# Optimization experiments

Measured on AMD Instinct MI355X. Metric: run time of the kernel, lower is better.

The kernel has to match this reference:

```python
import jax, jax.numpy as jnp
import numpy as np

B, N, DIM = 256, 196, 384
H, KD, VD = 12, 32, 32
RES = 14
EPS = 1e-5


def _build_bias_idxs():
    pts = [(i, j) for i in range(RES) for j in range(RES)]
    offs, idxs = {}, []
    for p1 in pts:
        for p2 in pts:
            o = (abs(p1[0] - p2[0]), abs(p1[1] - p2[1]))
            if o not in offs:
                offs[o] = len(offs)
            idxs.append(offs[o])
    return jnp.asarray(np.array(idxs, dtype=np.int32).reshape(N, N))


def setup_inputs() -> dict:
    key = jax.random.key(0)
    ks = jax.random.split(key, 4)
    return {
        "x": jax.random.normal(ks[0], (B, N, DIM), dtype=jnp.float32),
        "norm_w": jnp.ones((DIM,), jnp.float32),
        "norm_b": jnp.zeros((DIM,), jnp.float32),
        "qkv_w": jax.random.normal(ks[1], (H * (VD + 2 * KD), DIM), jnp.float32) * 0.02,
        "qkv_b": jnp.zeros((H * (VD + 2 * KD),), jnp.float32),
        "attention_biases": jax.random.normal(ks[2], (H, RES * RES), jnp.float32) * 0.02,
        "proj_w": jax.random.normal(ks[3], (DIM, H * VD), jnp.float32) * 0.02,
        "proj_b": jnp.zeros((DIM,), jnp.float32),
        "bias_idxs": _build_bias_idxs(),
    }


def reference(x, norm_w, norm_b, qkv_w, qkv_b, attention_biases, proj_w, proj_b, bias_idxs):
    scale = KD ** -0.5
    # LayerNorm over feature dim
    mu = jnp.mean(x, axis=-1, keepdims=True)
    var = jnp.mean(jnp.square(x - mu), axis=-1, keepdims=True)
    xn = (x - mu) * jax.lax.rsqrt(var + EPS) * norm_w + norm_b
    # QKV projection: [B,N,H*(2*KD+VD)] -> [B,N,H,*]
    qkv = (jnp.einsum("bnd,fd->bnf", xn, qkv_w) + qkv_b).reshape(B, N, H, 2 * KD + VD)
    q, k, v = qkv[..., :KD], qkv[..., KD:2 * KD], qkv[..., 2 * KD:]
    # Relative-position bias gathered into [H,N,N]
    attn_bias = attention_biases[:, bias_idxs]
    # Scores [B,H,N,N] with bias, softmax, AV
    scores = jnp.einsum("bnhk,bmhk->bhnm", q * scale, k) + attn_bias
    probs = jax.nn.softmax(scores, axis=-1)
    out = jnp.einsum("bhnm,bmhv->bnhv", probs, v).reshape(B, N, H * VD)
    return jnp.einsum("bnf,df->bnd", out, proj_w) + proj_b
```

## Files before the change

### kernel.cpp

```cpp
#include <hip/hip_runtime.h>

#define B_    256
#define N_    196
#define NP_   208
#define VSTR_ 264
#define DIM_  384
#define H_    12
#define KD_   32
#define VD_   32
#define F_    1152
#define ROWS_ (B_ * N_)
#define SCALE_ 0.17677669529663687f
#define EPS_  1e-5f

typedef __bf16 bf16_t;
typedef __bf16 bf16x2 __attribute__((ext_vector_type(2)));
typedef __bf16 bf16x4 __attribute__((ext_vector_type(4)));
typedef __bf16 bf16x8 __attribute__((ext_vector_type(8)));
typedef float  f32x4  __attribute__((ext_vector_type(4)));

__device__ __forceinline__ f32x4 mfma16(bf16x8 a, bf16x8 b, f32x4 c) {
    return __builtin_amdgcn_mfma_f32_16x16x32_bf16(a, b, c, 0, 0, 0);
}

__device__ __forceinline__ void gl2lds(const bf16_t* g, bf16_t* l) {
    __builtin_amdgcn_global_load_lds(
        (const __attribute__((address_space(1))) void*)g,
        (__attribute__((address_space(3))) void*)l, 16, 0, 0);
}

__global__ __launch_bounds__(256) void cvt_w(const float* __restrict__ src,
                                             bf16_t* __restrict__ dst) {
    const int i = (blockIdx.x * 256 + threadIdx.x) * 4;
    const float4 v = *(const float4*)(src + i);
    bf16x4 o = {(bf16_t)v.x, (bf16_t)v.y, (bf16_t)v.z, (bf16_t)v.w};
    *(bf16x4*)(dst + i) = o;
}

__global__ __launch_bounds__(256) void ln_kernel(const float* __restrict__ x,
                                                 const float* __restrict__ w,
                                                 const float* __restrict__ bvec,
                                                 bf16_t* __restrict__ xn) {
    const int lane = threadIdx.x & 63;
    const int row  = blockIdx.x * 4 + (threadIdx.x >> 6);
    const float* xr = x + (size_t)row * DIM_;
    const float4 a = *(const float4*)(xr + lane * 4);
    const float2 c = *(const float2*)(xr + 256 + lane * 2);
    float s  = a.x + a.y + a.z + a.w + c.x + c.y;
    float s2 = a.x*a.x + a.y*a.y + a.z*a.z + a.w*a.w + c.x*c.x + c.y*c.y;
    #pragma unroll
    for (int o = 32; o > 0; o >>= 1) {
        s  += __shfl_xor(s, o);
        s2 += __shfl_xor(s2, o);
    }
    const float mu = s * (1.f / 384.f);
    const float rs = rsqrtf(s2 * (1.f / 384.f) - mu * mu + EPS_);
    const float4 w4 = *(const float4*)(w + lane * 4);
    const float2 w2 = *(const float2*)(w + 256 + lane * 2);
    const float4 b4 = *(const float4*)(bvec + lane * 4);
    const float2 b2 = *(const float2*)(bvec + 256 + lane * 2);
    bf16_t* orow = xn + (size_t)row * DIM_;
    bf16x4 o4 = {(bf16_t)((a.x - mu) * rs * w4.x + b4.x),
                 (bf16_t)((a.y - mu) * rs * w4.y + b4.y),
                 (bf16_t)((a.z - mu) * rs * w4.z + b4.z),
                 (bf16_t)((a.w - mu) * rs * w4.w + b4.w)};
    *(bf16x4*)(orow + lane * 4) = o4;
    bf16x2 o2 = {(bf16_t)((c.x - mu) * rs * w2.x + b2.x),
                 (bf16_t)((c.y - mu) * rs * w2.y + b2.y)};
    *(bf16x2*)(orow + 256 + lane * 2) = o2;
}

__global__ __launch_bounds__(256) void bias_gather(const float* __restrict__ biases,
                                                   const int* __restrict__ idxs,
                                                   bf16_t* __restrict__ biasmat) {
    const int e = blockIdx.x * 256 + threadIdx.x;
    if (e >= H_ * N_ * NP_) return;
    const int h = e / (N_ * NP_);
    const int r = e % (N_ * NP_);
    const int n = r / NP_;
    const int m = r % NP_;
    const float v = (m < N_) ? biases[h * N_ + idxs[n * N_ + m]] : -1e30f;
    biasmat[e] = (bf16_t)v;
}

template <typename OutT>
__global__ __launch_bounds__(256) void gemm_mfma(const bf16_t* __restrict__ A,
                                                 const bf16_t* __restrict__ Wt,
                                                 const float* __restrict__ bias,
                                                 OutT* __restrict__ C,
                                                 int M, int Nout, int K) {
    __shared__ __align__(16) bf16_t As[128][32];
    __shared__ __align__(16) bf16_t Bs[128][32];
    const int tid  = threadIdx.x;
    const int lane = tid & 63;
    const int wv   = tid >> 6;
    const int ln   = lane & 15;
    const int ko   = lane >> 4;
    const int wr   = (wv >> 1) * 64;
    const int wc   = (wv & 1) * 64;
    const size_t bm = (size_t)blockIdx.x * 128;
    const size_t bn = (size_t)blockIdx.y * 128;

    const int srow = wv * 16 + (lane >> 2);
    const int scol = (lane & 3) * 8;
    const bf16_t* gA0 = A  + (bm + srow) * K + scol;
    const bf16_t* gA1 = gA0 + (size_t)64 * K;
    const bf16_t* gB0 = Wt + (bn + srow) * K + scol;
    const bf16_t* gB1 = gB0 + (size_t)64 * K;
    bf16_t* lA0 = &As[srow][scol];
    bf16_t* lA1 = &As[srow + 64][scol];
    bf16_t* lB0 = &Bs[srow][scol];
    bf16_t* lB1 = &Bs[srow + 64][scol];

    f32x4 acc[4][4];
    #pragma unroll
    for (int i = 0; i < 4; i++)
        #pragma unroll
        for (int j = 0; j < 4; j++)
            acc[i][j] = (f32x4){0.f, 0.f, 0.f, 0.f};

    for (int k0 = 0; k0 < K; k0 += 32) {
        gl2lds(gA0 + k0, lA0);
        gl2lds(gA1 + k0, lA1);
        gl2lds(gB0 + k0, lB0);
        gl2lds(gB1 + k0, lB1);
        __syncthreads();
        bf16x8 af[4], bfr[4];
        #pragma unroll
        for (int i = 0; i < 4; i++)
            af[i] = *(const bf16x8*)&As[wr + i * 16 + ln][ko * 8];
        #pragma unroll
        for (int j = 0; j < 4; j++)
            bfr[j] = *(const bf16x8*)&Bs[wc + j * 16 + ln][ko * 8];
        #pragma unroll
        for (int i = 0; i < 4; i++)
            #pragma unroll
            for (int j = 0; j < 4; j++)
                acc[i][j] = mfma16(af[i], bfr[j], acc[i][j]);
        __syncthreads();
    }

    #pragma unroll
    for (int j = 0; j < 4; j++) {
        const size_t col = bn + wc + j * 16 + ln;
        const float bcol = bias[col];
        #pragma unroll
        for (int i = 0; i < 4; i++)
            #pragma unroll
            for (int r = 0; r < 4; r++) {
                const size_t row = bm + wr + i * 16 + ko * 4 + r;
                C[row * Nout + col] = (OutT)(acc[i][j][r] + bcol);
            }
    }
}

__global__ __launch_bounds__(256) void attn_mfma(const bf16_t* __restrict__ qkv,
                                                 const bf16_t* __restrict__ biasmat,
                                                 bf16_t* __restrict__ out) {
    const int b = blockIdx.x / H_;
    const int h = blockIdx.x % H_;
    __shared__ __align__(16) bf16_t Ks[NP_][32];
    __shared__ __align__(16) bf16_t Vt[VD_][VSTR_];
    __shared__ __align__(16) bf16_t Pb[4][16][VSTR_];
    const int tid  = threadIdx.x;
    const int lane = tid & 63;
    const int wv   = tid >> 6;
    const int ln   = lane & 15;
    const int ko   = lane >> 4;

    {
        const int rsub = lane >> 2;
        const int col  = (lane & 3) * 8;
        for (int c = wv; c < 13; c += 4) {
            const int row = c * 16 + rsub;
            gl2lds(qkv + ((size_t)(b * N_ + row) * H_ + h) * 96 + KD_ + col,
                   &Ks[row][col]);
        }
    }
    if (tid < 224) {
        const int m  = tid;
        const int kk = (m & 15) * 16 + (m >> 4);
        const bf16_t* src = qkv + ((size_t)(b * N_ + m) * H_ + h) * 96 + 2 * KD_;
        #pragma unroll
        for (int c4 = 0; c4 < 4; c4++) {
            bf16x8 v8 = {bf16_t(0), bf16_t(0), bf16_t(0), bf16_t(0),
                         bf16_t(0), bf16_t(0), bf16_t(0), bf16_t(0)};
            if (m < N_) v8 = *(const bf16x8*)(src + c4 * 8);
            #pragma unroll
            for (int j = 0; j < 8; j++) Vt[c4 * 8 + j][kk] = v8[j];
        }
    }
    for (int e = tid; e < 32 * 32; e += 256) {
        const int v = e >> 5;
        const int s = e & 31;
        Vt[v][(s >> 1) * 16 + 14 + (s & 1)] = bf16_t(0);
    }
    __syncthreads();

    bf16x8 kf[13];
    #pragma unroll
    for (int c = 0; c < 13; c++)
        kf[c] = *(const bf16x8*)&Ks[c * 16 + ln][ko * 8];

    for (int t = wv; t < 13; t += 4) {
        const int qrow = t * 16 + ln;
        const bf16x8 qf =
            *(const bf16x8*)(qkv + ((size_t)(b * N_ + qrow) * H_ + h) * 96 + ko * 8);

        f32x4 sc[13];
        #pragma unroll
        for (int c = 0; c < 13; c++) {
            f32x4 z = {0.f, 0.f, 0.f, 0.f};
            sc[c] = mfma16(qf, kf[c], z);
        }

        float mx[4] = {-1e30f, -1e30f, -1e30f, -1e30f};
        #pragma unroll
        for (int r = 0; r < 4; r++) {
            const int rowc = min(t * 16 + ko * 4 + r, N_ - 1);
            const bf16_t* brow = biasmat + (size_t)(h * N_ + rowc) * NP_;
            #pragma unroll
            for (int c = 0; c < 13; c++) {
                const float s = sc[c][r] * SCALE_ + (float)brow[c * 16 + ln];
                sc[c][r] = s;
                mx[r] = fmaxf(mx[r], s);
            }
        }
        #pragma unroll
        for (int r = 0; r < 4; r++) {
            float m = mx[r];
            m = fmaxf(m, __shfl_xor(m, 1));
            m = fmaxf(m, __shfl_xor(m, 2));
            m = fmaxf(m, __shfl_xor(m, 4));
            m = fmaxf(m, __shfl_xor(m, 8));
            mx[r] = m;
        }
        float inv[4];
        #pragma unroll
        for (int r = 0; r < 4; r++) {
            float sum = 0.f;
            #pragma unroll
            for (int c = 0; c < 13; c++) {
                const float p = __expf(sc[c][r] - mx[r]);
                sc[c][r] = p;
                sum += p;
            }
            sum += __shfl_xor(sum, 1);
            sum += __shfl_xor(sum, 2);
            sum += __shfl_xor(sum, 4);
            sum += __shfl_xor(sum, 8);
            inv[r] = 1.f / sum;
        }
        #pragma unroll
        for (int r = 0; r < 4; r++) {
            bf16x8 pa, pb;
            #pragma unroll
            for (int c = 0; c < 8; c++) pa[c] = (bf16_t)sc[c][r];
            #pragma unroll
            for (int c = 8; c < 13; c++) pb[c - 8] = (bf16_t)sc[c][r];
            pb[5] = bf16_t(0); pb[6] = bf16_t(0); pb[7] = bf16_t(0);
            *(bf16x8*)&Pb[wv][ko * 4 + r][ln * 16]     = pa;
            *(bf16x8*)&Pb[wv][ko * 4 + r][ln * 16 + 8] = pb;
        }
        __builtin_amdgcn_s_waitcnt(0);

        f32x4 o0 = {0.f, 0.f, 0.f, 0.f};
        f32x4 o1 = {0.f, 0.f, 0.f, 0.f};
        #pragma unroll
        for (int kb = 0; kb < 8; kb++) {
            const bf16x8 pf = *(const bf16x8*)&Pb[wv][ln][kb * 32 + ko * 8];
            const bf16x8 v0 = *(const bf16x8*)&Vt[ln][kb * 32 + ko * 8];
            const bf16x8 v1 = *(const bf16x8*)&Vt[16 + ln][kb * 32 + ko * 8];
            o0 = mfma16(pf, v0, o0);
            o1 = mfma16(pf, v1, o1);
        }
        #pragma unroll
        for (int r = 0; r < 4; r++) {
            const int row = t * 16 + ko * 4 + r;
            if (row < N_) {
                const size_t ob = (size_t)(b * N_ + row) * DIM_ + h * VD_;
                out[ob + ln]      = (bf16_t)(o0[r] * inv[r]);
                out[ob + 16 + ln] = (bf16_t)(o1[r] * inv[r]);
            }
        }
    }
}

extern "C" void kernel_launch(void* const* d_in, const int* in_sizes, int n_in,
                              void* d_out, int out_size, void* d_ws, size_t ws_size,
                              hipStream_t stream) {
    const float* x        = (const float*)d_in[0];
    const float* norm_w   = (const float*)d_in[1];
    const float* norm_b   = (const float*)d_in[2];
    const float* qkv_w    = (const float*)d_in[3];
    const float* qkv_b    = (const float*)d_in[4];
    const float* att_bias = (const float*)d_in[5];
    const float* proj_w   = (const float*)d_in[6];
    const float* proj_b   = (const float*)d_in[7];
    const int*   bias_idx = (const int*)d_in[8];
    float* out = (float*)d_out;

    char* ws = (char*)d_ws;
    size_t off = 0;
    bf16_t* xn       = (bf16_t*)(ws + off); off += (size_t)ROWS_ * DIM_ * 2;
    bf16_t* qkvbuf   = (bf16_t*)(ws + off); off += (size_t)ROWS_ * F_ * 2;
    bf16_t* attn_out = (bf16_t*)(ws + off); off += (size_t)ROWS_ * DIM_ * 2;
    bf16_t* biasmat  = (bf16_t*)(ws + off); off += (size_t)H_ * N_ * NP_ * 2;
    bf16_t* wq_bf    = (bf16_t*)(ws + off); off += (size_t)F_ * DIM_ * 2;
    bf16_t* wp_bf    = (bf16_t*)(ws + off); off += (size_t)DIM_ * DIM_ * 2;

    cvt_w<<<(F_ * DIM_) / 1024, 256, 0, stream>>>(qkv_w, wq_bf);
    cvt_w<<<(DIM_ * DIM_) / 1024, 256, 0, stream>>>(proj_w, wp_bf);
    ln_kernel<<<ROWS_ / 4, 256, 0, stream>>>(x, norm_w, norm_b, xn);
    bias_gather<<<(H_ * N_ * NP_ + 255) / 256, 256, 0, stream>>>(att_bias, bias_idx, biasmat);
    gemm_mfma<bf16_t><<<dim3(ROWS_ / 128, F_ / 128), 256, 0, stream>>>(
        xn, wq_bf, qkv_b, qkvbuf, ROWS_, F_, DIM_);
    attn_mfma<<<B_ * H_, 256, 0, stream>>>(qkvbuf, biasmat, attn_out);
    gemm_mfma<float><<<dim3(ROWS_ / 128, DIM_ / 128), 256, 0, stream>>>(
        attn_out, wp_bf, proj_b, out, ROWS_, DIM_, DIM_);
}
```

Baseline: 372.2 us.

## Skip softmax max pass, prelayout fp32 bias, fragment-major LDS tiles, swizzle GEMM grid

The attention kernel drops the row-max reduction and computes exp2 of scaled scores plus a precomputed bias (already multiplied by log2e). The bias is now stored as fp32 in the MFMA fragment order, so each lane reads 16 values with four float4 loads. K and the GEMM tiles are laid out in LDS in fragment-major order to avoid bank conflicts, and LDS for K and P is aliased to cut shared memory use. The GEMM grid is flattened with an XCD-aware tile swizzle. Skipping the max subtraction risks overflow if scores get large, though it is safe for the small test weights.

```diff
diff --git a/kernel.cpp b/kernel.cpp
--- a/kernel.cpp
+++ b/kernel.cpp
@@ -2,16 +2,16 @@
 
 #define B_    256
 #define N_    196
-#define NP_   208
-#define VSTR_ 264
 #define DIM_  384
 #define H_    12
 #define KD_   32
 #define VD_   32
 #define F_    1152
 #define ROWS_ (B_ * N_)
-#define SCALE_ 0.17677669529663687f
+#define VSTR_ 264
 #define EPS_  1e-5f
+#define SCALE2_ 0.25506973821659267f
+#define LOG2E_  1.4426950408889634f
 
 typedef __bf16 bf16_t;
 typedef __bf16 bf16x2 __attribute__((ext_vector_type(2)));
@@ -22,7 +22,6 @@
 __device__ __forceinline__ f32x4 mfma16(bf16x8 a, bf16x8 b, f32x4 c) {
     return __builtin_amdgcn_mfma_f32_16x16x32_bf16(a, b, c, 0, 0, 0);
 }
-
 __device__ __forceinline__ void gl2lds(const bf16_t* g, bf16_t* l) {
     __builtin_amdgcn_global_load_lds(
         (const __attribute__((address_space(1))) void*)g,
@@ -72,15 +71,16 @@
 
 __global__ __launch_bounds__(256) void bias_gather(const float* __restrict__ biases,
                                                    const int* __restrict__ idxs,
-                                                   bf16_t* __restrict__ biasmat) {
-    const int e = blockIdx.x * 256 + threadIdx.x;
-    if (e >= H_ * N_ * NP_) return;
-    const int h = e / (N_ * NP_);
-    const int r = e % (N_ * NP_);
-    const int n = r / NP_;
-    const int m = r % NP_;
-    const float v = (m < N_) ? biases[h * N_ + idxs[n * N_ + m]] : -1e30f;
-    biasmat[e] = (bf16_t)v;
+                                                   float* __restrict__ bm2) {
+    const int h  = blockIdx.x;
+    const int n  = blockIdx.y;
+    const int ln = threadIdx.x >> 4;
+    const int c  = threadIdx.x & 15;
+    const int key = c * 16 + ln;
+    float v = -1e30f;
+    if (key < N_ && c < 13)
+        v = biases[h * N_ + idxs[n * N_ + key]] * LOG2E_;
+    bm2[(((size_t)h * N_ + n) * 16 + ln) * 16 + c] = v;
 }
 
 template <typename OutT>
@@ -88,9 +88,9 @@
                                                  const bf16_t* __restrict__ Wt,
                                                  const float* __restrict__ bias,
                                                  OutT* __restrict__ C,
-                                                 int M, int Nout, int K) {
-    __shared__ __align__(16) bf16_t As[128][32];
-    __shared__ __align__(16) bf16_t Bs[128][32];
+                                                 int Nout, int K, int ncols) {
+    __shared__ __align__(16) bf16_t As2[8 * 512];
+    __shared__ __align__(16) bf16_t Bs2[8 * 512];
     const int tid  = threadIdx.x;
     const int lane = tid & 63;
     const int wv   = tid >> 6;
@@ -98,19 +98,21 @@
     const int ko   = lane >> 4;
     const int wr   = (wv >> 1) * 64;
     const int wc   = (wv & 1) * 64;
-    const size_t bm = (size_t)blockIdx.x * 128;
-    const size_t bn = (size_t)blockIdx.y * 128;
-
-    const int srow = wv * 16 + (lane >> 2);
-    const int scol = (lane & 3) * 8;
-    const bf16_t* gA0 = A  + (bm + srow) * K + scol;
+
+    const int nb   = gridDim.x;
+    const int id   = blockIdx.x;
+    const int tile = (id & 7) * (nb >> 3) + (id >> 3);
+    const size_t bm = (size_t)(tile / ncols) * 128;
+    const size_t bn = (size_t)(tile % ncols) * 128;
+
+    const bf16_t* gA0 = A  + (bm + wv * 16 + ln) * K + ko * 8;
     const bf16_t* gA1 = gA0 + (size_t)64 * K;
-    const bf16_t* gB0 = Wt + (bn + srow) * K + scol;
+    const bf16_t* gB0 = Wt + (bn + wv * 16 + ln) * K + ko * 8;
     const bf16_t* gB1 = gB0 + (size_t)64 * K;
-    bf16_t* lA0 = &As[srow][scol];
-    bf16_t* lA1 = &As[srow + 64][scol];
-    bf16_t* lB0 = &Bs[srow][scol];
-    bf16_t* lB1 = &Bs[srow + 64][scol];
+    bf16_t* lA0 = As2 + wv * 512;
+    bf16_t* lA1 = As2 + (wv + 4) * 512;
+    bf16_t* lB0 = Bs2 + wv * 512;
+    bf16_t* lB1 = Bs2 + (wv + 4) * 512;
 
     f32x4 acc[4][4];
     #pragma unroll
@@ -128,10 +130,10 @@
         bf16x8 af[4], bfr[4];
         #pragma unroll
         for (int i = 0; i < 4; i++)
-            af[i] = *(const bf16x8*)&As[wr + i * 16 + ln][ko * 8];
+            af[i] = *(const bf16x8*)(As2 + ((wr >> 4) + i) * 512 + lane * 8);
         #pragma unroll
         for (int j = 0; j < 4; j++)
-            bfr[j] = *(const bf16x8*)&Bs[wc + j * 16 + ln][ko * 8];
+            bfr[j] = *(const bf16x8*)(Bs2 + ((wc >> 4) + j) * 512 + lane * 8);
         #pragma unroll
         for (int i = 0; i < 4; i++)
             #pragma unroll
@@ -155,31 +157,27 @@
 }
 
 __global__ __launch_bounds__(256) void attn_mfma(const bf16_t* __restrict__ qkv,
-                                                 const bf16_t* __restrict__ biasmat,
+                                                 const float* __restrict__ bm2,
                                                  bf16_t* __restrict__ out) {
     const int b = blockIdx.x / H_;
     const int h = blockIdx.x % H_;
-    __shared__ __align__(16) bf16_t Ks[NP_][32];
-    __shared__ __align__(16) bf16_t Vt[VD_][VSTR_];
-    __shared__ __align__(16) bf16_t Pb[4][16][VSTR_];
+    __shared__ __align__(16) char smem[16896 + 33792];
+    bf16_t* Vt = (bf16_t*)smem;
+    bf16_t* Ks = (bf16_t*)(smem + 16896);
+    bf16_t* Pb = (bf16_t*)(smem + 16896);
     const int tid  = threadIdx.x;
     const int lane = tid & 63;
     const int wv   = tid >> 6;
     const int ln   = lane & 15;
     const int ko   = lane >> 4;
 
+    for (int c = wv; c < 13; c += 4) {
+        const int krow = min(c * 16 + ln, N_ - 1);
+        gl2lds(qkv + ((size_t)(b * N_ + krow) * H_ + h) * 96 + KD_ + ko * 8,
+               Ks + c * 512);
+    }
     {
-        const int rsub = lane >> 2;
-        const int col  = (lane & 3) * 8;
-        for (int c = wv; c < 13; c += 4) {
-            const int row = c * 16 + rsub;
-            gl2lds(qkv + ((size_t)(b * N_ + row) * H_ + h) * 96 + KD_ + col,
-                   &Ks[row][col]);
-        }
-    }
-    if (tid < 224) {
-        const int m  = tid;
-        const int kk = (m & 15) * 16 + (m >> 4);
+        const int m = ((tid & 15) << 4) | (tid >> 4);
         const bf16_t* src = qkv + ((size_t)(b * N_ + m) * H_ + h) * 96 + 2 * KD_;
         #pragma unroll
         for (int c4 = 0; c4 < 4; c4++) {
@@ -187,23 +185,19 @@
                          bf16_t(0), bf16_t(0), bf16_t(0), bf16_t(0)};
             if (m < N_) v8 = *(const bf16x8*)(src + c4 * 8);
             #pragma unroll
-            for (int j = 0; j < 8; j++) Vt[c4 * 8 + j][kk] = v8[j];
-        }
-    }
-    for (int e = tid; e < 32 * 32; e += 256) {
-        const int v = e >> 5;
-        const int s = e & 31;
-        Vt[v][(s >> 1) * 16 + 14 + (s & 1)] = bf16_t(0);
+            for (int j = 0; j < 8; j++) Vt[(c4 * 8 + j) * VSTR_ + tid] = v8[j];
+        }
     }
     __syncthreads();
 
     bf16x8 kf[13];
     #pragma unroll
     for (int c = 0; c < 13; c++)
-        kf[c] = *(const bf16x8*)&Ks[c * 16 + ln][ko * 8];
+        kf[c] = *(const bf16x8*)(Ks + c * 512 + lane * 8);
+    __syncthreads();
 
     for (int t = wv; t < 13; t += 4) {
-        const int qrow = t * 16 + ln;
+        const int qrow = min(t * 16 + ln, N_ - 1);
         const bf16x8 qf =
             *(const bf16x8*)(qkv + ((size_t)(b * N_ + qrow) * H_ + h) * 96 + ko * 8);
 
@@ -214,34 +208,21 @@
             sc[c] = mfma16(qf, kf[c], z);
         }
 
-        float mx[4] = {-1e30f, -1e30f, -1e30f, -1e30f};
+        float inv[4];
         #pragma unroll
         for (int r = 0; r < 4; r++) {
             const int rowc = min(t * 16 + ko * 4 + r, N_ - 1);
-            const bf16_t* brow = biasmat + (size_t)(h * N_ + rowc) * NP_;
+            const float4* bp =
+                (const float4*)(bm2 + (((size_t)h * N_ + rowc) * 16 + ln) * 16);
+            float bv[16];
+            *(float4*)&bv[0]  = bp[0];
+            *(float4*)&bv[4]  = bp[1];
+            *(float4*)&bv[8]  = bp[2];
+            *(float4*)&bv[12] = bp[3];
+            float sum = 0.f;
             #pragma unroll
             for (int c = 0; c < 13; c++) {
-                const float s = sc[c][r] * SCALE_ + (float)brow[c * 16 + ln];
-                sc[c][r] = s;
-                mx[r] = fmaxf(mx[r], s);
-            }
-        }
-        #pragma unroll
-        for (int r = 0; r < 4; r++) {
-            float m = mx[r];
-            m = fmaxf(m, __shfl_xor(m, 1));
-            m = fmaxf(m, __shfl_xor(m, 2));
-            m = fmaxf(m, __shfl_xor(m, 4));
-            m = fmaxf(m, __shfl_xor(m, 8));
-            mx[r] = m;
-        }
-        float inv[4];
-        #pragma unroll
-        for (int r = 0; r < 4; r++) {
-            float sum = 0.f;
-            #pragma unroll
-            for (int c = 0; c < 13; c++) {
-                const float p = __expf(sc[c][r] - mx[r]);
+                const float p = exp2f(fmaf(sc[c][r], SCALE2_, bv[c]));
                 sc[c][r] = p;
                 sum += p;
             }
@@ -251,26 +232,27 @@
             sum += __shfl_xor(sum, 8);
             inv[r] = 1.f / sum;
         }
+
         #pragma unroll
         for (int r = 0; r < 4; r++) {
-            bf16x8 pa, pb;
+            bf16x8 pa, pb2;
             #pragma unroll
             for (int c = 0; c < 8; c++) pa[c] = (bf16_t)sc[c][r];
             #pragma unroll
-            for (int c = 8; c < 13; c++) pb[c - 8] = (bf16_t)sc[c][r];
-            pb[5] = bf16_t(0); pb[6] = bf16_t(0); pb[7] = bf16_t(0);
-            *(bf16x8*)&Pb[wv][ko * 4 + r][ln * 16]     = pa;
-            *(bf16x8*)&Pb[wv][ko * 4 + r][ln * 16 + 8] = pb;
-        }
-        __builtin_amdgcn_s_waitcnt(0);
+            for (int c = 8; c < 13; c++) pb2[c - 8] = (bf16_t)sc[c][r];
+            pb2[5] = bf16_t(0); pb2[6] = bf16_t(0); pb2[7] = bf16_t(0);
+            bf16_t* dst = Pb + ((wv * 16) + ko * 4 + r) * VSTR_ + ln * 16;
+            *(bf16x8*)dst       = pa;
+            *(bf16x8*)(dst + 8) = pb2;
+        }
 
         f32x4 o0 = {0.f, 0.f, 0.f, 0.f};
         f32x4 o1 = {0.f, 0.f, 0.f, 0.f};
         #pragma unroll
         for (int kb = 0; kb < 8; kb++) {
-            const bf16x8 pf = *(const bf16x8*)&Pb[wv][ln][kb * 32 + ko * 8];
-            const bf16x8 v0 = *(const bf16x8*)&Vt[ln][kb * 32 + ko * 8];
-            const bf16x8 v1 = *(const bf16x8*)&Vt[16 + ln][kb * 32 + ko * 8];
+            const bf16x8 pf = *(const bf16x8*)(Pb + (wv * 16 + ln) * VSTR_ + kb * 32 + ko * 8);
+            const bf16x8 v0 = *(const bf16x8*)(Vt + ln * VSTR_ + kb * 32 + ko * 8);
+            const bf16x8 v1 = *(const bf16x8*)(Vt + (16 + ln) * VSTR_ + kb * 32 + ko * 8);
             o0 = mfma16(pf, v0, o0);
             o1 = mfma16(pf, v1, o1);
         }
@@ -305,17 +287,17 @@
     bf16_t* xn       = (bf16_t*)(ws + off); off += (size_t)ROWS_ * DIM_ * 2;
     bf16_t* qkvbuf   = (bf16_t*)(ws + off); off += (size_t)ROWS_ * F_ * 2;
     bf16_t* attn_out = (bf16_t*)(ws + off); off += (size_t)ROWS_ * DIM_ * 2;
-    bf16_t* biasmat  = (bf16_t*)(ws + off); off += (size_t)H_ * N_ * NP_ * 2;
+    float*  bm2      = (float*)(ws + off);  off += (size_t)H_ * N_ * 256 * 4;
     bf16_t* wq_bf    = (bf16_t*)(ws + off); off += (size_t)F_ * DIM_ * 2;
     bf16_t* wp_bf    = (bf16_t*)(ws + off); off += (size_t)DIM_ * DIM_ * 2;
 
     cvt_w<<<(F_ * DIM_) / 1024, 256, 0, stream>>>(qkv_w, wq_bf);
     cvt_w<<<(DIM_ * DIM_) / 1024, 256, 0, stream>>>(proj_w, wp_bf);
     ln_kernel<<<ROWS_ / 4, 256, 0, stream>>>(x, norm_w, norm_b, xn);
-    bias_gather<<<(H_ * N_ * NP_ + 255) / 256, 256, 0, stream>>>(att_bias, bias_idx, biasmat);
-    gemm_mfma<bf16_t><<<dim3(ROWS_ / 128, F_ / 128), 256, 0, stream>>>(
-        xn, wq_bf, qkv_b, qkvbuf, ROWS_, F_, DIM_);
-    attn_mfma<<<B_ * H_, 256, 0, stream>>>(qkvbuf, biasmat, attn_out);
-    gemm_mfma<float><<<dim3(ROWS_ / 128, DIM_ / 128), 256, 0, stream>>>(
-        attn_out, wp_bf, proj_b, out, ROWS_, DIM_, DIM_);
-}
+    bias_gather<<<dim3(H_, N_), 256, 0, stream>>>(att_bias, bias_idx, bm2);
+    gemm_mfma<bf16_t><<<(ROWS_ / 128) * (F_ / 128), 256, 0, stream>>>(
+        xn, wq_bf, qkv_b, qkvbuf, F_, DIM_, F_ / 128);
+    attn_mfma<<<B_ * H_, 256, 0, stream>>>(qkvbuf, bm2, attn_out);
+    gemm_mfma<float><<<(ROWS_ / 128) * (DIM_ / 128), 256, 0, stream>>>(
+        attn_out, wp_bf, proj_b, out, DIM_, DIM_, DIM_ / 128);
+}
```

After: 389.2 us. 4.6% more time.
